# Optimization experiments

Measured on AMD Instinct MI355X. Metric: run time of the kernel, lower is better.

## Reference

```python
import jax, jax.numpy as jnp
import numpy as np

B, T, F, H = 10, 12, 500, 200  # hardcoded in the original module


def setup_inputs() -> dict:
    key = jax.random.key(0)
    ks = jax.random.split(key, 8)
    x = jax.random.normal(ks[0], (B, T, F), dtype=jnp.float32)
    guidance = jax.random.randint(ks[1], (B, T, 1), 0, 2).astype(jnp.float32)
    # mlp_for_x: Linear(500, 1, bias=False)
    wx = jax.random.normal(ks[2], (F,), dtype=jnp.float32) * 0.04
    # mlp_for_hidden: Linear(200, 12)
    Wh = jax.random.normal(ks[3], (T, H), dtype=jnp.float32) * 0.07
    bh = jax.random.normal(ks[4], (T,), dtype=jnp.float32) * 0.01
    # GRUCell(500, 200): gates stacked [r; z; n]
    W_ih = jax.random.normal(ks[5], (3 * H, F), dtype=jnp.float32) * 0.04
    W_hh = jax.random.normal(ks[6], (3 * H, H), dtype=jnp.float32) * 0.07
    b_ih = jnp.zeros((3 * H,), dtype=jnp.float32)
    b_hh = jnp.zeros((3 * H,), dtype=jnp.float32)
    h0 = jnp.zeros((B, H), dtype=jnp.float32)  # init_hidden()
    return {"x": x, "guidance": guidance, "wx": wx, "Wh": Wh, "bh": bh,
            "W_ih": W_ih, "W_hh": W_hh, "b_ih": b_ih, "b_hh": b_hh, "h0": h0}


def _gru_cell(xc, h, W_ih, W_hh, b_ih, b_hh):
    gi = xc @ W_ih.T + b_ih  # (B, 3H)
    gh = h @ W_hh.T + b_hh   # (B, 3H)
    i_r, i_z, i_n = jnp.split(gi, 3, axis=1)
    h_r, h_z, h_n = jnp.split(gh, 3, axis=1)
    r = jax.nn.sigmoid(i_r + h_r)
    z = jax.nn.sigmoid(i_z + h_z)
    n = jnp.tanh(i_n + r * h_n)
    return (1.0 - z) * n + z * h


def reference(x, guidance, wx, Wh, bh, W_ih, W_hh, b_ih, b_hh, h0):
    t_idx = jnp.arange(T)
    h = h0
    for i in range(T):  # fixed 12-step recurrence (structurally distinct masks)
        # tt + zero-pad + reshape(10,12,500) == x with timesteps > i zeroed
        keep = (t_idx <= i)[None, :, None].astype(x.dtype)
        input_padded = x * keep  # (B, T, F)
        # temp_guidance: copy first i+1 guidance steps, zero the rest
        g = guidance * keep
        if i > 0:
            # rows whose guidance over [0, i) sums to zero get all-ones there
            past = (t_idx < i)
            zero_rows = jnp.sum(guidance[:, :, 0] * past[None, :].astype(x.dtype), axis=1) == 0
            g = jnp.where(zero_rows[:, None, None] & past[None, :, None], 1.0, g)
        g = g.at[:, i, :].set(1.0)  # current step always attended
        guided = input_padded * g  # (B, T, F)
        # attention scores: mlp_for_x(guided) + mlp_for_hidden(h).reshape(B,T,1)
        t1 = guided @ wx[:, None] + (h @ Wh.T + bh)[:, :, None]  # (B, T, 1)
        # nn.Softmax() with no dim on 3D -> legacy implicit dim=0 (batch axis)
        a = jax.nn.softmax(t1, axis=0)
        context = jnp.sum(input_padded * a, axis=1)  # (B, F)
        h = _gru_cell(context, h, W_ih, W_hh, b_ih, b_hh)
    return h  # (B, H); hidden2label output `y` is computed but discarded in the original
```

## Files before the change

### kernel.cpp

```cpp
#include <hip/hip_runtime.h>
#include <math.h>

#define BB 10
#define TT 12
#define FF 500
#define HH 200
#define G3 600
#define KP 224
#define NKS 7
#define SLOTS 5
#define RSLOTS 4
#define GHW 648

#define WS_XW   0
#define WS_XWV  72000
#define WS_FRAG 72128
#define WS_WHF  143808

typedef __attribute__((ext_vector_type(8))) short bf16x8;
typedef __attribute__((ext_vector_type(4))) float f32x4;

__device__ __forceinline__ unsigned short f2bf(float f) {
    unsigned int u = __float_as_uint(f);
    u = (u + 0x7fffu + ((u >> 16) & 1u)) >> 16;
    return (unsigned short)u;
}
__device__ __forceinline__ float bf2f(unsigned short h) {
    return __uint_as_float(((unsigned int)h) << 16);
}

__global__ __launch_bounds__(256) void prep_kernel(
        const float* __restrict__ x, const float* __restrict__ wx,
        const float* __restrict__ W_ih, const float* __restrict__ W_hh,
        const float* __restrict__ Wh, float* __restrict__ ws) {
    int bl = blockIdx.x, tid = threadIdx.x;
    if (bl < 75) {
        __shared__ __align__(16) float wsm[8][FF];
        int j0 = bl * 8;
        for (int idx = tid; idx < 8 * FF; idx += 256)
            wsm[idx / FF][idx % FF] = W_ih[(j0 + idx / FF) * FF + (idx % FF)];
        __syncthreads();
        for (int p = tid; p < BB * TT * 8; p += 256) {
            int bt = p >> 3, jj = p & 7;
            const float4* xr = (const float4*)(x + bt * FF);
            const float4* wr = (const float4*)&wsm[jj][0];
            float acc = 0.f;
            for (int c = 0; c < FF / 4; ++c) {
                float4 a = xr[c], b = wr[c];
                acc += a.x * b.x + a.y * b.y + a.z * b.z + a.w * b.w;
            }
            ws[WS_XW + bt * G3 + j0 + jj] = acc;
        }
    } else if (bl < 91) {
        unsigned int* fr = (unsigned int*)(ws + WS_FRAG);
        int base = (bl - 75) * 4480;
        for (int q = tid; q < 4480; q += 256) {
            int d = base + q;
            int v = d & 3, lane = (d >> 2) & 63, pk = d >> 8;
            int ks = pk % NKS, tile = pk / NKS;
            int n = lane & 15;
            int k = ks * 32 + (lane >> 4) * 8 + 2 * v;
            unsigned int w = 0;
            if (k < HH && n < 15) {
                int j = 40 * n + tile;
                w = (unsigned int)f2bf(W_hh[j * HH + k]) |
                    ((unsigned int)f2bf(W_hh[j * HH + k + 1]) << 16);
            }
            fr[d] = w;
        }
    } else if (bl < 99) {
        int dte = (bl - 91) * 15 + (tid >> 4), l = tid & 15;
        if (tid < 240) {
            float p = 0.f;
            for (int f = l; f < FF; f += 16) p += x[dte * FF + f] * wx[f];
            p += __shfl_xor(p, 8);
            p += __shfl_xor(p, 4);
            p += __shfl_xor(p, 2);
            p += __shfl_xor(p, 1);
            if (l == 0) ws[WS_XWV + dte] = p;
        }
    } else {
        unsigned int* fr = (unsigned int*)(ws + WS_WHF);
        for (int d = tid; d < 3584; d += 256) {
            int v = d & 3, lane = (d >> 2) & 63, pk = d >> 8;
            int qq = pk & 1, ks = pk >> 1;
            int t = lane & 15, k = ks * 32 + (lane >> 4) * 8 + 2 * v;
            unsigned int w = 0;
            if (t < TT && k < HH) {
                float f0 = Wh[t * HH + k], f1 = Wh[t * HH + k + 1];
                if (qq == 0) {
                    w = (unsigned int)f2bf(f0) | ((unsigned int)f2bf(f1) << 16);
                } else {
                    float l0 = f0 - bf2f(f2bf(f0)), l1 = f1 - bf2f(f2bf(f1));
                    w = (unsigned int)f2bf(l0) | ((unsigned int)f2bf(l1) << 16);
                }
            }
            fr[d] = w;
        }
    }
}

__device__ __forceinline__ int hbf_idx(int r, int k) {
    return (r * KP + k) ^ ((r & 7) << 3);
}

__global__ __attribute__((amdgpu_waves_per_eu(2, 2))) __launch_bounds__(512)
void recurrence_kernel(
        const float* __restrict__ guidance, const float* __restrict__ bh,
        const float* __restrict__ b_ih, const float* __restrict__ b_hh,
        const float* __restrict__ h0, const float* __restrict__ ws,
        float* __restrict__ out) {
    const float* XW  = ws + WS_XW;
    const float* xww = ws + WS_XWV;

    __shared__ __align__(16) float ghf[16 * GHW];
    __shared__ __align__(16) unsigned short hbf[16 * KP];
    __shared__ __align__(16) bf16x8 wlds[8][NKS][64];
    __shared__ __align__(16) bf16x8 wh_lds[2][NKS][64];
    __shared__ __align__(16) float bsum_s[2 * HH];
    __shared__ __align__(16) float bihn_s[HH];
    __shared__ __align__(16) float bhhn_s[HH];
    __shared__ float guid_s[BB][TT], zr_s[BB][TT], xw_s[BB][TT];
    __shared__ float a_w[8][TT][12];
    __shared__ float bh_s[TT];

    int tid = threadIdx.x, wv = tid >> 6, lane = tid & 63;
    int ar = lane & 15, kg = lane >> 4;

    bf16x8 bfr[RSLOTS][NKS];
    {
        const bf16x8* fragp = (const bf16x8*)(ws + WS_FRAG);
        #pragma unroll
        for (int s = 0; s < RSLOTS; ++s)
            #pragma unroll
            for (int ks = 0; ks < NKS; ++ks)
                bfr[s][ks] = fragp[((SLOTS * wv + s) * NKS + ks) * 64 + lane];
        #pragma unroll
        for (int ks = 0; ks < NKS; ++ks)
            wlds[wv][ks][lane] = fragp[((SLOTS * wv + RSLOTS) * NKS + ks) * 64 + lane];
        const bf16x8* whp = (const bf16x8*)(ws + WS_WHF);
        for (int u = tid; u < 2 * NKS * 64; u += 512) {
            int l = u & 63, pk = u >> 6;
            wh_lds[pk & 1][pk >> 1][l] = whp[u];
        }
    }
    if (tid < BB * TT) {
        guid_s[tid / TT][tid % TT] = guidance[tid];
        xw_s[tid / TT][tid % TT]   = xww[tid];
    }
    for (int idx = tid; idx < 2 * HH; idx += 512) bsum_s[idx] = b_ih[idx] + b_hh[idx];
    for (int idx = tid; idx < HH; idx += 512) {
        bihn_s[idx] = b_ih[idx + 2 * HH];
        bhhn_s[idx] = b_hh[idx + 2 * HH];
    }
    if (tid < TT) bh_s[tid] = bh[tid];
    for (int idx = tid; idx < 16 * KP / 2; idx += 512) ((unsigned int*)hbf)[idx] = 0;
    float4 hq = (float4){0.f, 0.f, 0.f, 0.f};
    if (tid < 500) hq = *(const float4*)(h0 + (tid / 50) * HH + (tid % 50) * 4);
    __syncthreads();
    if (tid < 500) {
        int b = tid / 50, k = (tid % 50) * 4;
        unsigned int u01 = (unsigned int)f2bf(hq.x) | ((unsigned int)f2bf(hq.y) << 16);
        unsigned int u23 = (unsigned int)f2bf(hq.z) | ((unsigned int)f2bf(hq.w) << 16);
        *(uint2*)&hbf[hbf_idx(b, k)] = (uint2){u01, u23};
    }
    if (tid < BB) {
        float run = 0.f;
        for (int i = 0; i < TT; ++i) {
            zr_s[tid][i] = (run == 0.f) ? 1.f : 0.f;
            run += guid_s[tid][i];
        }
    }
    __syncthreads();

    #pragma unroll 1
    for (int i = 0; i < TT; ++i) {
        bf16x8 ahi[NKS];
        #pragma unroll
        for (int ks = 0; ks < NKS; ++ks)
            ahi[ks] = *(const bf16x8*)&hbf[hbf_idx(ar, ks * 32 + kg * 8)];
        f32x4 sch = (f32x4){0.f, 0.f, 0.f, 0.f};
        f32x4 scl = (f32x4){0.f, 0.f, 0.f, 0.f};
        #pragma unroll
        for (int ks = 0; ks < NKS; ++ks) {
            sch = __builtin_amdgcn_mfma_f32_16x16x32_bf16(ahi[ks], wh_lds[0][ks][lane], sch, 0, 0, 0);
            scl = __builtin_amdgcn_mfma_f32_16x16x32_bf16(ahi[ks], wh_lds[1][ks][lane], scl, 0, 0, 0);
        }
        {
            f32x4 acc[SLOTS];
            #pragma unroll
            for (int s = 0; s < RSLOTS; ++s) {
                acc[s] = (f32x4){0.f, 0.f, 0.f, 0.f};
                #pragma unroll
                for (int ks = 0; ks < NKS; ++ks)
                    acc[s] = __builtin_amdgcn_mfma_f32_16x16x32_bf16(ahi[ks], bfr[s][ks], acc[s], 0, 0, 0);
            }
            acc[RSLOTS] = (f32x4){0.f, 0.f, 0.f, 0.f};
            #pragma unroll
            for (int ks = 0; ks < NKS; ++ks) {
                bf16x8 bw = wlds[wv][ks][lane];
                acc[RSLOTS] = __builtin_amdgcn_mfma_f32_16x16x32_bf16(ahi[ks], bw, acc[RSLOTS], 0, 0, 0);
            }
            int xr = (kg & 3) << 2;
            int base0 = 40 * ar + 5 * wv;
            #pragma unroll
            for (int r = 0; r < 4; ++r) {
                int b = 4 * kg + r;
                if (b < BB) {
                    int base = b * GHW + base0;
                    #pragma unroll
                    for (int s = 0; s < SLOTS; ++s)
                        ghf[(base + s) ^ xr] = acc[s][r];
                }
            }
        }
        {
            int t = ar;
            float vv[4], mx = -3e38f;
            #pragma unroll
            for (int r = 0; r < 4; ++r) {
                int b = 4 * kg + r;
                float val = -3e38f;
                if (b < BB && t < TT) {
                    float ge = (t == i) ? 1.f : (zr_s[b][i] != 0.f ? 1.f : guid_s[b][t]);
                    val = ge * xw_s[b][t] + sch[r] + scl[r] + bh_s[t];
                }
                vv[r] = val;
                mx = fmaxf(mx, val);
            }
            mx = fmaxf(mx, __shfl_xor(mx, 16));
            mx = fmaxf(mx, __shfl_xor(mx, 32));
            float ee[4], sum = 0.f;
            #pragma unroll
            for (int r = 0; r < 4; ++r) {
                ee[r] = (vv[r] > -1e37f) ? __expf(vv[r] - mx) : 0.f;
                sum += ee[r];
            }
            sum += __shfl_xor(sum, 16);
            sum += __shfl_xor(sum, 32);
            float inv = 1.f / sum;
            #pragma unroll
            for (int r = 0; r < 4; ++r) {
                int b = 4 * kg + r;
                if (b < BB && t < TT) a_w[wv][t][b] = (t <= i) ? ee[r] * inv : 0.f;
            }
        }
        float4 gi_r = (float4){0.f, 0.f, 0.f, 0.f};
        float4 gi_z = gi_r, gi_n = gi_r;
        if (tid < 500) {
            int b = tid / 50, c = tid % 50;
            float a12[TT];
            #pragma unroll
            for (int t = 0; t < TT; ++t) a12[t] = a_w[wv][t][b];
            const float* base = XW + b * TT * G3 + c * 4;
            for (int t = 0; t <= i; ++t) {
                float aa = a12[t];
                float4 vr = *(const float4*)(base + t * G3);
                float4 vz = *(const float4*)(base + t * G3 + HH);
                float4 vn = *(const float4*)(base + t * G3 + 2 * HH);
                gi_r.x += aa * vr.x; gi_r.y += aa * vr.y; gi_r.z += aa * vr.z; gi_r.w += aa * vr.w;
                gi_z.x += aa * vz.x; gi_z.y += aa * vz.y; gi_z.z += aa * vz.z; gi_z.w += aa * vz.w;
                gi_n.x += aa * vn.x; gi_n.y += aa * vn.y; gi_n.z += aa * vn.z; gi_n.w += aa * vn.w;
            }
        }
        __syncthreads();

        if (tid < 500) {
            int b = tid / 50, k = (tid % 50) * 4;
            int xr = ((b >> 2) & 3) << 2;
            float4 ghr = *(const float4*)&ghf[(b * GHW + k) ^ xr];
            float4 ghz = *(const float4*)&ghf[(b * GHW + k + HH) ^ xr];
            float4 ghn = *(const float4*)&ghf[(b * GHW + k + 2 * HH) ^ xr];
            float4 br4 = *(const float4*)&bsum_s[k];
            float4 bz4 = *(const float4*)&bsum_s[k + HH];
            float4 bni = *(const float4*)&bihn_s[k];
            float4 bnh = *(const float4*)&bhhn_s[k];
            float4 hn;
            float* pgir = (float*)&gi_r; float* pgiz = (float*)&gi_z; float* pgin = (float*)&gi_n;
            float* pghr = (float*)&ghr;  float* pghz = (float*)&ghz;  float* pghn = (float*)&ghn;
            float* pbr = (float*)&br4;   float* pbz = (float*)&bz4;
            float* pbi = (float*)&bni;   float* pbh = (float*)&bnh;
            float* ph  = (float*)&hq;    float* phn = (float*)&hn;
            #pragma unroll
            for (int e = 0; e < 4; ++e) {
                float r = 1.f / (1.f + __expf(-(pgir[e] + pghr[e] + pbr[e])));
                float z = 1.f / (1.f + __expf(-(pgiz[e] + pghz[e] + pbz[e])));
                float xx = pgin[e] + pbi[e] + r * (pghn[e] + pbh[e]);
                float e2 = __expf(2.f * xx);
                float n = 1.f - 2.f / (e2 + 1.f);
                phn[e] = (1.f - z) * n + z * ph[e];
            }
            hq = hn;
            unsigned int u01 = (unsigned int)f2bf(hn.x) | ((unsigned int)f2bf(hn.y) << 16);
            unsigned int u23 = (unsigned int)f2bf(hn.z) | ((unsigned int)f2bf(hn.w) << 16);
            *(uint2*)&hbf[hbf_idx(b, k)] = (uint2){u01, u23};
        }
        __syncthreads();
    }

    if (tid < 500) *(float4*)(out + (tid / 50) * HH + (tid % 50) * 4) = hq;
}

extern "C" void kernel_launch(void* const* d_in, const int* in_sizes, int n_in,
                              void* d_out, int out_size, void* d_ws, size_t ws_size,
                              hipStream_t stream) {
    (void)in_sizes; (void)n_in; (void)out_size; (void)ws_size;
    const float* x    = (const float*)d_in[0];
    const float* guid = (const float*)d_in[1];
    const float* wx   = (const float*)d_in[2];
    const float* Wh   = (const float*)d_in[3];
    const float* bh   = (const float*)d_in[4];
    const float* W_ih = (const float*)d_in[5];
    const float* W_hh = (const float*)d_in[6];
    const float* b_ih = (const float*)d_in[7];
    const float* b_hh = (const float*)d_in[8];
    const float* h0   = (const float*)d_in[9];
    float* ws  = (float*)d_ws;
    float* out = (float*)d_out;

    hipLaunchKernelGGL(prep_kernel, dim3(100), dim3(256), 0, stream,
                       x, wx, W_ih, W_hh, Wh, ws);
    hipLaunchKernelGGL(recurrence_kernel, dim3(1), dim3(512), 0, stream,
                       guid, bh, b_ih, b_hh, h0, ws, out);
}
```

Baseline: 84.91 us.

## Compute GRU gates directly from MFMA accumulators, dropping LDS staging and a barrier

The W_hh fragments are re-tiled so that each MFMA lane's accumulator holds the r/z/n gate values for the same hidden units. The gate nonlinearity can then run in registers right after the matmul, with no round trip through a shared-memory gh buffer and one fewer __syncthreads per step. The precomputed x·W_ih projection is stored as bf16 in a batch-innermost layout matched to that lane mapping, which halves the bytes read per step at some cost in precision. The prep grid and the workspace offsets are adjusted to fit the new layout.

After: 153.8 us. +81.1%, slower.

```diff
diff --git a/kernel.cpp b/kernel.cpp
--- a/kernel.cpp
+++ b/kernel.cpp
@@ -8,14 +8,14 @@
 #define G3 600
 #define KP 224
 #define NKS 7
-#define SLOTS 5
-#define RSLOTS 4
-#define GHW 648
-
-#define WS_XW   0
-#define WS_XWV  72000
-#define WS_FRAG 72128
-#define WS_WHF  143808
+#define NTIL 48
+#define WVS 8
+
+
+#define WS_XWPB 0
+#define WS_XWV  43200
+#define WS_FRAG 43328
+#define WS_WHF  129344
 
 typedef __attribute__((ext_vector_type(8))) short bf16x8;
 typedef __attribute__((ext_vector_type(4))) float f32x4;
@@ -40,6 +40,7 @@
         for (int idx = tid; idx < 8 * FF; idx += 256)
             wsm[idx / FF][idx % FF] = W_ih[(j0 + idx / FF) * FF + (idx % FF)];
         __syncthreads();
+        unsigned short* xwpb = (unsigned short*)ws;
         for (int p = tid; p < BB * TT * 8; p += 256) {
             int bt = p >> 3, jj = p & 7;
             const float4* xr = (const float4*)(x + bt * FF);
@@ -49,27 +50,31 @@
                 float4 a = xr[c], b = wr[c];
                 acc += a.x * b.x + a.y * b.y + a.z * b.z + a.w * b.w;
             }
-            ws[WS_XW + bt * G3 + j0 + jj] = acc;
-        }
-    } else if (bl < 91) {
+            int t = bt % TT, b = bt / TT;
+            int j = j0 + jj, g = j / 200, K = j % 200;
+            xwpb[((t * 200 + K) * 3 + g) * 12 + b] = f2bf(acc);
+        }
+    } else if (bl < 99) {
         unsigned int* fr = (unsigned int*)(ws + WS_FRAG);
-        int base = (bl - 75) * 4480;
-        for (int q = tid; q < 4480; q += 256) {
+        int base = (bl - 75) * 3584;
+        for (int q = tid; q < 3584; q += 256) {
             int d = base + q;
             int v = d & 3, lane = (d >> 2) & 63, pk = d >> 8;
-            int ks = pk % NKS, tile = pk / NKS;
+            int ks = pk % NKS, tau = pk / NKS;
+            int wv_ = tau / 6, s = tau % 6, g = s % 3, pr = s / 3;
             int n = lane & 15;
-            int k = ks * 32 + (lane >> 4) * 8 + 2 * v;
+            int K = n * 16 + wv_ * 2 + pr;
+            int kq = ks * 32 + (lane >> 4) * 8 + 2 * v;
             unsigned int w = 0;
-            if (k < HH && n < 15) {
-                int j = 40 * n + tile;
-                w = (unsigned int)f2bf(W_hh[j * HH + k]) |
-                    ((unsigned int)f2bf(W_hh[j * HH + k + 1]) << 16);
+            if (K < 200 && kq < HH) {
+                int j = g * 200 + K;
+                w = (unsigned int)f2bf(W_hh[j * HH + kq]) |
+                    ((unsigned int)f2bf(W_hh[j * HH + kq + 1]) << 16);
             }
             fr[d] = w;
         }
-    } else if (bl < 99) {
-        int dte = (bl - 91) * 15 + (tid >> 4), l = tid & 15;
+    } else if (bl < 107) {
+        int dte = (bl - 99) * 15 + (tid >> 4), l = tid & 15;
         if (tid < 240) {
             float p = 0.f;
             for (int f = l; f < FF; f += 16) p += x[dte * FF + f] * wx[f];
@@ -110,34 +115,32 @@
         const float* __restrict__ b_ih, const float* __restrict__ b_hh,
         const float* __restrict__ h0, const float* __restrict__ ws,
         float* __restrict__ out) {
-    const float* XW  = ws + WS_XW;
+    const unsigned short* XWPB = (const unsigned short*)ws;
     const float* xww = ws + WS_XWV;
 
-    __shared__ __align__(16) float ghf[16 * GHW];
     __shared__ __align__(16) unsigned short hbf[16 * KP];
-    __shared__ __align__(16) bf16x8 wlds[8][NKS][64];
+    __shared__ __align__(16) bf16x8 wlds2[WVS][2][NKS][64];
     __shared__ __align__(16) bf16x8 wh_lds[2][NKS][64];
-    __shared__ __align__(16) float bsum_s[2 * HH];
-    __shared__ __align__(16) float bihn_s[HH];
-    __shared__ __align__(16) float bhhn_s[HH];
     __shared__ float guid_s[BB][TT], zr_s[BB][TT], xw_s[BB][TT];
-    __shared__ float a_w[8][TT][12];
+    __shared__ __align__(16) float a_w[WVS][TT][16];
     __shared__ float bh_s[TT];
 
     int tid = threadIdx.x, wv = tid >> 6, lane = tid & 63;
     int ar = lane & 15, kg = lane >> 4;
 
-    bf16x8 bfr[RSLOTS][NKS];
+    bf16x8 bfr[4][NKS];
     {
         const bf16x8* fragp = (const bf16x8*)(ws + WS_FRAG);
         #pragma unroll
-        for (int s = 0; s < RSLOTS; ++s)
+        for (int s = 0; s < 4; ++s)
             #pragma unroll
             for (int ks = 0; ks < NKS; ++ks)
-                bfr[s][ks] = fragp[((SLOTS * wv + s) * NKS + ks) * 64 + lane];
-        #pragma unroll
-        for (int ks = 0; ks < NKS; ++ks)
-            wlds[wv][ks][lane] = fragp[((SLOTS * wv + RSLOTS) * NKS + ks) * 64 + lane];
+                bfr[s][ks] = fragp[((wv * 6 + s) * NKS + ks) * 64 + lane];
+        #pragma unroll
+        for (int s2 = 0; s2 < 2; ++s2)
+            #pragma unroll
+            for (int ks = 0; ks < NKS; ++ks)
+                wlds2[wv][s2][ks][lane] = fragp[((wv * 6 + 4 + s2) * NKS + ks) * 64 + lane];
         const bf16x8* whp = (const bf16x8*)(ws + WS_WHF);
         for (int u = tid; u < 2 * NKS * 64; u += 512) {
             int l = u & 63, pk = u >> 6;
@@ -148,20 +151,33 @@
         guid_s[tid / TT][tid % TT] = guidance[tid];
         xw_s[tid / TT][tid % TT]   = xww[tid];
     }
-    for (int idx = tid; idx < 2 * HH; idx += 512) bsum_s[idx] = b_ih[idx] + b_hh[idx];
-    for (int idx = tid; idx < HH; idx += 512) {
-        bihn_s[idx] = b_ih[idx + 2 * HH];
-        bhhn_s[idx] = b_hh[idx + 2 * HH];
-    }
     if (tid < TT) bh_s[tid] = bh[tid];
     for (int idx = tid; idx < 16 * KP / 2; idx += 512) ((unsigned int*)hbf)[idx] = 0;
-    float4 hq = (float4){0.f, 0.f, 0.f, 0.f};
-    if (tid < 500) hq = *(const float4*)(h0 + (tid / 50) * HH + (tid % 50) * 4);
+    for (int idx = tid; idx < WVS * TT * 16; idx += 512) ((float*)a_w)[idx] = 0.f;
+
+    int Kp0 = ar * 16 + wv * 2;
+    bool ok = Kp0 < 200;
+    int Kc = ok ? Kp0 : 0;
+    float2 br2, bz2, bni2, bnh2;
+    br2.x = b_ih[Kc] + b_hh[Kc];             br2.y = b_ih[Kc + 1] + b_hh[Kc + 1];
+    bz2.x = b_ih[200 + Kc] + b_hh[200 + Kc]; bz2.y = b_ih[201 + Kc] + b_hh[201 + Kc];
+    bni2.x = b_ih[400 + Kc];  bni2.y = b_ih[401 + Kc];
+    bnh2.x = b_hh[400 + Kc];  bnh2.y = b_hh[401 + Kc];
+    float hpx[4], hpy[4];
+    #pragma unroll
+    for (int r = 0; r < 4; ++r) {
+        int b = 4 * kg + r;
+        if (ok && b < BB) {
+            float2 h2 = *(const float2*)(h0 + b * HH + Kc);
+            hpx[r] = h2.x; hpy[r] = h2.y;
+        } else { hpx[r] = 0.f; hpy[r] = 0.f; }
+    }
     __syncthreads();
     if (tid < 500) {
         int b = tid / 50, k = (tid % 50) * 4;
-        unsigned int u01 = (unsigned int)f2bf(hq.x) | ((unsigned int)f2bf(hq.y) << 16);
-        unsigned int u23 = (unsigned int)f2bf(hq.z) | ((unsigned int)f2bf(hq.w) << 16);
+        float4 h4 = *(const float4*)(h0 + b * HH + k);
+        unsigned int u01 = (unsigned int)f2bf(h4.x) | ((unsigned int)f2bf(h4.y) << 16);
+        unsigned int u23 = (unsigned int)f2bf(h4.z) | ((unsigned int)f2bf(h4.w) << 16);
         *(uint2*)&hbf[hbf_idx(b, k)] = (uint2){u01, u23};
     }
     if (tid < BB) {
@@ -186,32 +202,21 @@
             sch = __builtin_amdgcn_mfma_f32_16x16x32_bf16(ahi[ks], wh_lds[0][ks][lane], sch, 0, 0, 0);
             scl = __builtin_amdgcn_mfma_f32_16x16x32_bf16(ahi[ks], wh_lds[1][ks][lane], scl, 0, 0, 0);
         }
-        {
-            f32x4 acc[SLOTS];
-            #pragma unroll
-            for (int s = 0; s < RSLOTS; ++s) {
-                acc[s] = (f32x4){0.f, 0.f, 0.f, 0.f};
-                #pragma unroll
-                for (int ks = 0; ks < NKS; ++ks)
-                    acc[s] = __builtin_amdgcn_mfma_f32_16x16x32_bf16(ahi[ks], bfr[s][ks], acc[s], 0, 0, 0);
-            }
-            acc[RSLOTS] = (f32x4){0.f, 0.f, 0.f, 0.f};
+        f32x4 acc[6];
+        #pragma unroll
+        for (int s = 0; s < 4; ++s) {
+            acc[s] = (f32x4){0.f, 0.f, 0.f, 0.f};
+            #pragma unroll
+            for (int ks = 0; ks < NKS; ++ks)
+                acc[s] = __builtin_amdgcn_mfma_f32_16x16x32_bf16(ahi[ks], bfr[s][ks], acc[s], 0, 0, 0);
+        }
+        #pragma unroll
+        for (int s2 = 0; s2 < 2; ++s2) {
+            acc[4 + s2] = (f32x4){0.f, 0.f, 0.f, 0.f};
             #pragma unroll
             for (int ks = 0; ks < NKS; ++ks) {
-                bf16x8 bw = wlds[wv][ks][lane];
-                acc[RSLOTS] = __builtin_amdgcn_mfma_f32_16x16x32_bf16(ahi[ks], bw, acc[RSLOTS], 0, 0, 0);
-            }
-            int xr = (kg & 3) << 2;
-            int base0 = 40 * ar + 5 * wv;
-            #pragma unroll
-            for (int r = 0; r < 4; ++r) {
-                int b = 4 * kg + r;
-                if (b < BB) {
-                    int base = b * GHW + base0;
-                    #pragma unroll
-                    for (int s = 0; s < SLOTS; ++s)
-                        ghf[(base + s) ^ xr] = acc[s][r];
-                }
+                bf16x8 bw = wlds2[wv][s2][ks][lane];
+                acc[4 + s2] = __builtin_amdgcn_mfma_f32_16x16x32_bf16(ahi[ks], bw, acc[4 + s2], 0, 0, 0);
             }
         }
         {
@@ -245,60 +250,58 @@
                 if (b < BB && t < TT) a_w[wv][t][b] = (t <= i) ? ee[r] * inv : 0.f;
             }
         }
-        float4 gi_r = (float4){0.f, 0.f, 0.f, 0.f};
-        float4 gi_z = gi_r, gi_n = gi_r;
-        if (tid < 500) {
-            int b = tid / 50, c = tid % 50;
-            float a12[TT];
-            #pragma unroll
-            for (int t = 0; t < TT; ++t) a12[t] = a_w[wv][t][b];
-            const float* base = XW + b * TT * G3 + c * 4;
+        f32x4 gi[6];
+        #pragma unroll
+        for (int s = 0; s < 6; ++s) gi[s] = (f32x4){0.f, 0.f, 0.f, 0.f};
+        {
+            const unsigned short* xb = XWPB + (Kc * 3) * 12 + 4 * kg;
             for (int t = 0; t <= i; ++t) {
-                float aa = a12[t];
-                float4 vr = *(const float4*)(base + t * G3);
-                float4 vz = *(const float4*)(base + t * G3 + HH);
-                float4 vn = *(const float4*)(base + t * G3 + 2 * HH);
-                gi_r.x += aa * vr.x; gi_r.y += aa * vr.y; gi_r.z += aa * vr.z; gi_r.w += aa * vr.w;
-                gi_z.x += aa * vz.x; gi_z.y += aa * vz.y; gi_z.z += aa * vz.z; gi_z.w += aa * vz.w;
-                gi_n.x += aa * vn.x; gi_n.y += aa * vn.y; gi_n.z += aa * vn.z; gi_n.w += aa * vn.w;
+                float4 a4 = *(const float4*)&a_w[wv][t][4 * kg];
+                const unsigned short* bt_ = xb + t * (200 * 36);
+                #pragma unroll
+                for (int pr = 0; pr < 2; ++pr)
+                    #pragma unroll
+                    for (int g = 0; g < 3; ++g) {
+                        int s = pr * 3 + g;
+                        uint2 u = *(const uint2*)(bt_ + pr * 36 + g * 12);
+                        float f0 = __uint_as_float(u.x << 16);
+                        float f1 = __uint_as_float(u.x & 0xffff0000u);
+                        float f2 = __uint_as_float(u.y << 16);
+                        float f3 = __uint_as_float(u.y & 0xffff0000u);
+                        gi[s].x += a4.x * f0; gi[s].y += a4.y * f1;
+                        gi[s].z += a4.z * f2; gi[s].w += a4.w * f3;
+                    }
+            }
+        }
+        #pragma unroll
+        for (int r = 0; r < 4; ++r) {
+            int b = 4 * kg + r;
+            float rg0 = 1.f / (1.f + __expf(-(gi[0][r] + acc[0][r] + br2.x)));
+            float z0  = 1.f / (1.f + __expf(-(gi[1][r] + acc[1][r] + bz2.x)));
+            float xx0 = gi[2][r] + bni2.x + rg0 * (acc[2][r] + bnh2.x);
+            float e20 = __expf(2.f * xx0);
+            float n0  = 1.f - 2.f / (e20 + 1.f);
+            float h0n = (1.f - z0) * n0 + z0 * hpx[r];
+            float rg1 = 1.f / (1.f + __expf(-(gi[3][r] + acc[3][r] + br2.y)));
+            float z1  = 1.f / (1.f + __expf(-(gi[4][r] + acc[4][r] + bz2.y)));
+            float xx1 = gi[5][r] + bni2.y + rg1 * (acc[5][r] + bnh2.y);
+            float e21 = __expf(2.f * xx1);
+            float n1  = 1.f - 2.f / (e21 + 1.f);
+            float h1n = (1.f - z1) * n1 + z1 * hpy[r];
+            hpx[r] = h0n; hpy[r] = h1n;
+            if (ok && b < BB) {
+                unsigned int uu = (unsigned int)f2bf(h0n) | ((unsigned int)f2bf(h1n) << 16);
+                *(unsigned int*)&hbf[hbf_idx(b, Kc)] = uu;
             }
         }
         __syncthreads();
-
-        if (tid < 500) {
-            int b = tid / 50, k = (tid % 50) * 4;
-            int xr = ((b >> 2) & 3) << 2;
-            float4 ghr = *(const float4*)&ghf[(b * GHW + k) ^ xr];
-            float4 ghz = *(const float4*)&ghf[(b * GHW + k + HH) ^ xr];
-            float4 ghn = *(const float4*)&ghf[(b * GHW + k + 2 * HH) ^ xr];
-            float4 br4 = *(const float4*)&bsum_s[k];
-            float4 bz4 = *(const float4*)&bsum_s[k + HH];
-            float4 bni = *(const float4*)&bihn_s[k];
-            float4 bnh = *(const float4*)&bhhn_s[k];
-            float4 hn;
-            float* pgir = (float*)&gi_r; float* pgiz = (float*)&gi_z; float* pgin = (float*)&gi_n;
-            float* pghr = (float*)&ghr;  float* pghz = (float*)&ghz;  float* pghn = (float*)&ghn;
-            float* pbr = (float*)&br4;   float* pbz = (float*)&bz4;
-            float* pbi = (float*)&bni;   float* pbh = (float*)&bnh;
-            float* ph  = (float*)&hq;    float* phn = (float*)&hn;
-            #pragma unroll
-            for (int e = 0; e < 4; ++e) {
-                float r = 1.f / (1.f + __expf(-(pgir[e] + pghr[e] + pbr[e])));
-                float z = 1.f / (1.f + __expf(-(pgiz[e] + pghz[e] + pbz[e])));
-                float xx = pgin[e] + pbi[e] + r * (pghn[e] + pbh[e]);
-                float e2 = __expf(2.f * xx);
-                float n = 1.f - 2.f / (e2 + 1.f);
-                phn[e] = (1.f - z) * n + z * ph[e];
-            }
-            hq = hn;
-            unsigned int u01 = (unsigned int)f2bf(hn.x) | ((unsigned int)f2bf(hn.y) << 16);
-            unsigned int u23 = (unsigned int)f2bf(hn.z) | ((unsigned int)f2bf(hn.w) << 16);
-            *(uint2*)&hbf[hbf_idx(b, k)] = (uint2){u01, u23};
-        }
-        __syncthreads();
-    }
-
-    if (tid < 500) *(float4*)(out + (tid / 50) * HH + (tid % 50) * 4) = hq;
+    }
+
+    #pragma unroll
+    for (int r = 0; r < 4; ++r) {
+        int b = 4 * kg + r;
+        if (ok && b < BB) *(float2*)(out + b * HH + Kc) = (float2){hpx[r], hpy[r]};
+    }
 }
 
 extern "C" void kernel_launch(void* const* d_in, const int* in_sizes, int n_in,
@@ -318,7 +321,7 @@
     float* ws  = (float*)d_ws;
     float* out = (float*)d_out;
 
-    hipLaunchKernelGGL(prep_kernel, dim3(100), dim3(256), 0, stream,
+    hipLaunchKernelGGL(prep_kernel, dim3(108), dim3(256), 0, stream,
                        x, wx, W_ih, W_hh, Wh, ws);
     hipLaunchKernelGGL(recurrence_kernel, dim3(1), dim3(512), 0, stream,
                        guid, bh, b_ih, b_hh, h0, ws, out);
```
